# Kernel tuning notes

Hardware: AMD Instinct MI355X
Metric: run time of the kernel (lower is better)

Reference implementation:

```python
import jax, jax.numpy as jnp
import numpy as np

B, S, IN_F = 2, 2048, 1024
HEADS, DPH, OUT_F = 8, 64, 1024
ROOT_D = DPH ** 0.5


def setup_inputs() -> dict:
    key = jax.random.key(0)
    k1, k2, k3, k4, k5 = jax.random.split(key, 5)
    scale = 0.02
    return {
        "inputs": jax.random.normal(k1, (B, S, IN_F), dtype=jnp.float32),
        "Wq": jax.random.normal(k2, (IN_F, HEADS * DPH), dtype=jnp.float32) * scale,
        "Wk": jax.random.normal(k3, (IN_F, HEADS * DPH), dtype=jnp.float32) * scale,
        "Wv": jax.random.normal(k4, (IN_F, HEADS * DPH), dtype=jnp.float32) * scale,
        "Wo": jax.random.normal(k5, (DPH, OUT_F), dtype=jnp.float32) * scale,
        "bo": jnp.zeros((OUT_F,), dtype=jnp.float32),
    }


def reference(inputs, Wq, Wk, Wv, Wo, bo):
    b = inputs.shape[0]
    # Faithful to torch: raw view(b, heads, -1, d) reshape (NOT a transpose).
    q = (inputs @ Wq).reshape(b, HEADS, -1, DPH)  # [b, h, s, d]
    k = (inputs @ Wk).reshape(b, HEADS, -1, DPH)
    v = (inputs @ Wv).reshape(b, HEADS, -1, DPH)
    scores = jnp.einsum("bhqd,bhkd->bhqk", q, k)  # no pre-softmax scale
    attn = jax.nn.softmax(scores, axis=-1) / ROOT_D  # post-softmax scale (quirk)
    ctx = jnp.einsum("bhqk,bhkd->bhqd", attn, v)  # [b, h, s, d]
    # Per-head output projection d -> out_features; dropout p=0 is identity.
    return ctx @ Wo + bo  # [b, h, s, out_features]
```

## Files before the change

### kernel.cpp

```cpp
#include <hip/hip_runtime.h>


using short8  = __attribute__((ext_vector_type(8))) short;
using short4v = __attribute__((ext_vector_type(4))) short;
using f32x4   = __attribute__((ext_vector_type(4))) float;
using float4v = __attribute__((ext_vector_type(4))) float;
using uint4v  = __attribute__((ext_vector_type(4))) unsigned int;

__device__ __forceinline__ unsigned short f2bf(float x) {
  unsigned int u = __float_as_uint(x);
  u += 0x7FFFu + ((u >> 16) & 1u);
  return (unsigned short)(u >> 16);
}

#define GLD_LDS16(g, s)                                                              \
  __builtin_amdgcn_global_load_lds((const __attribute__((address_space(1))) unsigned int*)(g), \
                                   (__attribute__((address_space(3))) unsigned int*)(s), 16, 0, 0)

__global__ __launch_bounds__(256) void k_cvt(const float* __restrict__ in,
                                             unsigned short* __restrict__ out,
                                             int n4) {
  int id = blockIdx.x * 256 + threadIdx.x;
  if (id >= n4) return;
  float4v v = *(const float4v*)(in + (size_t)id * 4);
  short4v o;
#pragma unroll
  for (int i = 0; i < 4; ++i) o[i] = (short)f2bf(v[i]);
  *(short4v*)(out + (size_t)id * 4) = o;
}

__global__ __launch_bounds__(256) void k_twt3(const float* __restrict__ Wq,
                                              const float* __restrict__ Wk,
                                              const float* __restrict__ Wv,
                                              unsigned short* __restrict__ WT) {
  __shared__ alignas(16) unsigned short t[64][72];
  const int z = blockIdx.z;
  const float* W = (z == 0) ? Wq : (z == 1) ? Wk : Wv;
  unsigned short* dst0 = WT + (size_t)z * 524288;
  const int k0 = blockIdx.x * 64, n0 = blockIdx.y * 64;
  const int kk = threadIdx.x & 63, g = (threadIdx.x >> 6) * 16;
  const float* src = W + (size_t)(k0 + kk) * 512 + n0 + g;
#pragma unroll
  for (int j4 = 0; j4 < 4; ++j4) {
    float4v v = *(const float4v*)(src + j4 * 4);
#pragma unroll
    for (int i = 0; i < 4; ++i) t[g + j4 * 4 + i][kk] = f2bf(v[i]);
  }
  __syncthreads();
  const int nn = threadIdx.x >> 2, kg = (threadIdx.x & 3) * 16;
  short8 o0, o1;
#pragma unroll
  for (int j = 0; j < 8; ++j) { o0[j] = t[nn][kg + j]; o1[j] = t[nn][kg + 8 + j]; }
  unsigned short* dst = dst0 + (size_t)(n0 + nn) * 1024 + k0 + kg;
  *(short8*)dst = o0;
  *(short8*)(dst + 8) = o1;
}

__global__ __launch_bounds__(256) void k_twtO(const float* __restrict__ W,
                                              unsigned short* __restrict__ WT) {
  __shared__ alignas(16) unsigned short t[64][72];
  const int n0 = blockIdx.y * 64;
  const int kk = threadIdx.x & 63, g = (threadIdx.x >> 6) * 16;
  const float* src = W + (size_t)kk * 1024 + n0 + g;
#pragma unroll
  for (int j4 = 0; j4 < 4; ++j4) {
    float4v v = *(const float4v*)(src + j4 * 4);
#pragma unroll
    for (int i = 0; i < 4; ++i) t[g + j4 * 4 + i][kk] = f2bf(v[i]);
  }
  __syncthreads();
  const int nn = threadIdx.x >> 2, kg = (threadIdx.x & 3) * 16;
  short8 o0, o1;
#pragma unroll
  for (int j = 0; j < 8; ++j) { o0[j] = t[nn][kg + j]; o1[j] = t[nn][kg + 8 + j]; }
  unsigned short* dst = WT + (size_t)(n0 + nn) * 64 + kg;
  *(short8*)dst = o0;
  *(short8*)(dst + 8) = o1;
}

__global__ __launch_bounds__(256) void k_tv(const unsigned short* __restrict__ Vb,
                                            unsigned short* __restrict__ VT) {
  __shared__ alignas(16) unsigned short t[64][72];
  const int bh = blockIdx.y, r0 = blockIdx.x * 64;
  const int rr = threadIdx.x & 63, g = (threadIdx.x >> 6) * 16;
  const unsigned short* src = Vb + (size_t)bh * 131072 + (size_t)(r0 + rr) * 64 + g;
  short8 a = *(const short8*)src;
  short8 b = *(const short8*)(src + 8);
#pragma unroll
  for (int j = 0; j < 8; ++j) { t[g + j][rr] = a[j]; t[g + 8 + j][rr] = b[j]; }
  __syncthreads();
  const int d = threadIdx.x >> 2, rg = (threadIdx.x & 3) * 16;
  short8 o0, o1;
#pragma unroll
  for (int j = 0; j < 8; ++j) { o0[j] = t[d][rg + j]; o1[j] = t[d][rg + 8 + j]; }
  unsigned short* dst = VT + (size_t)bh * 131072 + (size_t)(r0 >> 6) * 4096 + d * 64 + rg;
  *(short8*)dst = o0;
  *(short8*)(dst + 8) = o1;
}

__global__ __launch_bounds__(256) void k_gemmqkv(const unsigned short* __restrict__ A,
                                                 const unsigned short* __restrict__ WT,
                                                 unsigned short* __restrict__ Q,
                                                 unsigned short* __restrict__ K_,
                                                 unsigned short* __restrict__ V_) {
  __shared__ alignas(16) unsigned short As[2][4096];
  __shared__ alignas(16) unsigned short Bs[2][8192];
  const int tid = threadIdx.x, w = tid >> 6, l = tid & 63;
  const int lr = l & 15, lg = l >> 4;
  const int m0 = blockIdx.x * 64;
  const int yy = blockIdx.y;
  const int wr = w >> 1, wc = w & 1;
  const unsigned short* ga = A  + (size_t)(m0 + w * 16 + (l >> 3)) * 1024 + (l & 7) * 8;
  const unsigned short* gb = WT + (size_t)(yy * 128 + w * 32 + (l >> 3)) * 1024 + (l & 7) * 8;

#pragma unroll
  for (int n = 0; n < 2; ++n) GLD_LDS16(ga + n * 8192, &As[0][w * 1024 + n * 512]);
#pragma unroll
  for (int n = 0; n < 4; ++n) GLD_LDS16(gb + n * 8192, &Bs[0][w * 2048 + n * 512]);
  asm volatile("s_waitcnt vmcnt(0)" ::: "memory");
  __syncthreads();

  f32x4 acc[2][4] = {};
  int cur = 0;
  for (int kt = 0; kt < 16; ++kt) {
    if (kt < 15) {
      const int k0 = (kt + 1) * 64;
#pragma unroll
      for (int n = 0; n < 2; ++n) GLD_LDS16(ga + n * 8192 + k0, &As[cur ^ 1][w * 1024 + n * 512]);
#pragma unroll
      for (int n = 0; n < 4; ++n) GLD_LDS16(gb + n * 8192 + k0, &Bs[cur ^ 1][w * 2048 + n * 512]);
    }
#pragma unroll
    for (int kk = 0; kk < 2; ++kk) {
      short8 a[2], b[4];
#pragma unroll
      for (int mi = 0; mi < 2; ++mi)
        a[mi] = *(const short8*)&As[cur][(wr * 32 + mi * 16 + lr) * 64 + kk * 32 + lg * 8];
#pragma unroll
      for (int ni = 0; ni < 4; ++ni)
        b[ni] = *(const short8*)&Bs[cur][(wc * 64 + ni * 16 + lr) * 64 + kk * 32 + lg * 8];
#pragma unroll
      for (int mi = 0; mi < 2; ++mi)
#pragma unroll
        for (int ni = 0; ni < 4; ++ni)
          acc[mi][ni] = __builtin_amdgcn_mfma_f32_16x16x32_bf16(a[mi], b[ni], acc[mi][ni], 0, 0, 0);
    }
    asm volatile("s_waitcnt vmcnt(0)" ::: "memory");
    __syncthreads();
    cur ^= 1;
  }
  const int which = yy >> 2;
  unsigned short* C = (which == 0) ? Q : (which == 1) ? K_ : V_;
  const int cbase = (yy & 3) * 128 + wc * 64;
#pragma unroll
  for (int mi = 0; mi < 2; ++mi)
#pragma unroll
    for (int ni = 0; ni < 4; ++ni) {
      int row = m0 + wr * 32 + mi * 16 + lg * 4;
      int col = cbase + ni * 16 + lr;
#pragma unroll
      for (int r = 0; r < 4; ++r)
        C[(size_t)(row + r) * 512 + col] = f2bf(acc[mi][ni][r]);
    }
}

__global__ __launch_bounds__(512) void k_attn(const unsigned short* __restrict__ Qb,
                                              const unsigned short* __restrict__ Kb,
                                              const unsigned short* __restrict__ VT,
                                              unsigned short* __restrict__ ctx) {
  __shared__ alignas(16) unsigned short Ks[2][8192];
  __shared__ alignas(16) unsigned short Vs[2][8192];
  __shared__ alignas(16) unsigned short Plds[8][16][128];
  const int tid = threadIdx.x, w = tid >> 6, l = tid & 63;
  const int lr = l & 15, lg = l >> 4;
  const int bid = blockIdx.x;
  const int xcd = bid & 7, j = bid >> 3;
  const int bh = xcd * 2 + (j >> 4);
  const int q0 = (j & 15) * 128;
  const int qrow = q0 + w * 16;
  const unsigned short* Qh  = Qb + (size_t)bh * 131072;
  const unsigned short* Kh  = Kb + (size_t)bh * 131072;
  const unsigned short* VTh = VT + (size_t)bh * 131072;

  short8 qb0 = *(const short8*)&Qh[(size_t)(qrow + lr) * 64 + lg * 8];
  short8 qb1 = *(const short8*)&Qh[(size_t)(qrow + lr) * 64 + 32 + lg * 8];

  const int srow = w * 8 + (l >> 3);
  const int scol = (((l & 7) ^ ((l >> 3) & 7)) << 3);
  const unsigned short* kps = Kh  + (size_t)srow * 64 + scol;
  const unsigned short* vps = VTh + (size_t)srow * 64 + scol;

#define STAGE(buf, it)                                                         \
  {                                                                            \
    _Pragma("unroll")                                                          \
    for (int sub = 0; sub < 2; ++sub) {                                        \
      GLD_LDS16(kps + (size_t)(2 * (it) + sub) * 4096, &Ks[buf][sub * 4096 + w * 512]); \
      GLD_LDS16(vps + (size_t)(2 * (it) + sub) * 4096, &Vs[buf][sub * 4096 + w * 512]); \
    }                                                                          \
  }

  f32x4 O[4] = {};
  float m_i = -1e30f, l_i = 0.f;

  STAGE(0, 0);
  asm volatile("s_waitcnt vmcnt(0)" ::: "memory");
  __syncthreads();

  const int fcol = ((lg ^ (lr & 7)) << 3);
  char* prow = (char*)&Plds[w][lr][0];
  int cur = 0;
  for (int it = 0; it < 16; ++it) {
    if (it < 15) STAGE(cur ^ 1, it + 1);
    f32x4 s[8] = {};
#pragma unroll
    for (int t = 0; t < 8; ++t) {
      const unsigned short* kRow = &Ks[cur][(t >> 2) * 4096 + ((t & 3) * 16 + lr) * 64];
      short8 ka = *(const short8*)(kRow + fcol);
      short8 kc = *(const short8*)(kRow + (fcol ^ 32));
      s[t] = __builtin_amdgcn_mfma_f32_16x16x32_bf16(ka, qb0, s[t], 0, 0, 0);
      s[t] = __builtin_amdgcn_mfma_f32_16x16x32_bf16(kc, qb1, s[t], 0, 0, 0);
    }
    short8 vf[4][4];
#pragma unroll
    for (int f = 0; f < 4; ++f) {
      const char* vRow0 = (const char*)&Vs[cur][(f * 16 + lr) * 64];
#pragma unroll
      for (int ks = 0; ks < 4; ++ks) {
        int ch = (((ks & 1) * 4 + lg) ^ (lr & 7));
        vf[f][ks] = *(const short8*)(vRow0 + (ks >> 1) * 8192 + ch * 16);
      }
    }
    float tm[8];
#pragma unroll
    for (int t = 0; t < 8; ++t)
      tm[t] = fmaxf(fmaxf(s[t][0], s[t][1]), fmaxf(s[t][2], s[t][3]));
    float tmax = fmaxf(fmaxf(fmaxf(tm[0], tm[1]), fmaxf(tm[2], tm[3])),
                       fmaxf(fmaxf(tm[4], tm[5]), fmaxf(tm[6], tm[7])));
    tmax = fmaxf(tmax, __shfl_xor(tmax, 16));
    tmax = fmaxf(tmax, __shfl_xor(tmax, 32));
    float mnew  = fmaxf(m_i, tmax);
    float alpha = __expf(m_i - mnew);
    float p[8][4];
#pragma unroll
    for (int t = 0; t < 8; ++t)
#pragma unroll
      for (int r = 0; r < 4; ++r) p[t][r] = __expf(s[t][r] - mnew);
    float us[8];
#pragma unroll
    for (int t = 0; t < 8; ++t)
      us[t] = (p[t][0] + p[t][1]) + (p[t][2] + p[t][3]);
    float ls = ((us[0] + us[1]) + (us[2] + us[3])) + ((us[4] + us[5]) + (us[6] + us[7]));
    ls += __shfl_xor(ls, 16);
    ls += __shfl_xor(ls, 32);
    l_i = l_i * alpha + ls;
    m_i = mnew;
#pragma unroll
    for (int f = 0; f < 4; ++f) O[f] *= alpha;
#pragma unroll
    for (int t = 0; t < 8; ++t) {
      short4v pk;
#pragma unroll
      for (int r = 0; r < 4; ++r) pk[r] = (short)f2bf(p[t][r]);
      int ch = ((2 * t + (lg >> 1)) ^ (lr & 7));
      *(short4v*)(prow + ch * 16 + (lg & 1) * 8) = pk;
    }
    asm volatile("s_waitcnt lgkmcnt(0)" ::: "memory");
    __builtin_amdgcn_sched_barrier(0);
    short8 pb[4];
#pragma unroll
    for (int ks = 0; ks < 4; ++ks)
      pb[ks] = *(const short8*)(prow + (((ks * 4 + lg) ^ (lr & 7)) << 4));
#pragma unroll
    for (int ks = 0; ks < 4; ++ks)
#pragma unroll
      for (int f = 0; f < 4; ++f)
        O[f] = __builtin_amdgcn_mfma_f32_16x16x32_bf16(vf[f][ks], pb[ks], O[f], 0, 0, 0);
    if (it < 15) {
      asm volatile("s_waitcnt vmcnt(0)" ::: "memory");
      __syncthreads();
    }
    cur ^= 1;
  }
  const float scale = 0.125f / l_i;
  unsigned short* base = ctx + (size_t)(bh * 2048 + qrow + lr) * 64;
#pragma unroll
  for (int f = 0; f < 4; ++f) {
    short4v o;
#pragma unroll
    for (int r = 0; r < 4; ++r) o[r] = (short)f2bf(O[f][r] * scale);
    *(short4v*)(base + f * 16 + lg * 4) = o;
  }
}

__global__ __launch_bounds__(256) void k_gemmo(const unsigned short* __restrict__ A,
                                               const unsigned short* __restrict__ BT,
                                               const float* __restrict__ bias,
                                               float* __restrict__ C) {
  __shared__ alignas(16) unsigned short As[128 * 64];
  __shared__ alignas(16) unsigned short Bs[128 * 64];
  const int tid = threadIdx.x, w = tid >> 6, l = tid & 63;
  const int lr = l & 15, lg = l >> 4;
  const int m0 = blockIdx.x * 128, n0 = blockIdx.y * 128;
  const int wr = w >> 1, wc = w & 1;
  const int srow = w * 8 + (l >> 3);
  const int scol = (l & 7) * 8;
  const unsigned short* ga = A  + (size_t)(m0 + srow) * 64 + scol;
  const unsigned short* gb = BT + (size_t)(n0 + srow) * 64 + scol;
#pragma unroll
  for (int i = 0; i < 4; ++i) {
    GLD_LDS16(ga + (size_t)i * 2048, As + (i * 32 + w * 8) * 64);
    GLD_LDS16(gb + (size_t)i * 2048, Bs + (i * 32 + w * 8) * 64);
  }
  asm volatile("s_waitcnt vmcnt(0)" ::: "memory");
  __syncthreads();
  f32x4 acc[4][4] = {};
#pragma unroll
  for (int kk = 0; kk < 2; ++kk) {
    short8 a[4], b[4];
#pragma unroll
    for (int mi = 0; mi < 4; ++mi)
      a[mi] = *(const short8*)&As[(wr * 64 + mi * 16 + lr) * 64 + kk * 32 + lg * 8];
#pragma unroll
    for (int ni = 0; ni < 4; ++ni)
      b[ni] = *(const short8*)&Bs[(wc * 64 + ni * 16 + lr) * 64 + kk * 32 + lg * 8];
#pragma unroll
    for (int mi = 0; mi < 4; ++mi)
#pragma unroll
      for (int ni = 0; ni < 4; ++ni)
        acc[mi][ni] = __builtin_amdgcn_mfma_f32_16x16x32_bf16(a[mi], b[ni], acc[mi][ni], 0, 0, 0);
  }
  float bv[4];
#pragma unroll
  for (int ni = 0; ni < 4; ++ni) bv[ni] = bias[n0 + wc * 64 + ni * 16 + lr];
#pragma unroll
  for (int mi = 0; mi < 4; ++mi)
#pragma unroll
    for (int ni = 0; ni < 4; ++ni) {
      int row = m0 + wr * 64 + mi * 16 + lg * 4;
      int col = n0 + wc * 64 + ni * 16 + lr;
#pragma unroll
      for (int r = 0; r < 4; ++r)
        C[(size_t)(row + r) * 1024 + col] = acc[mi][ni][r] + bv[ni];
    }
}

extern "C" void kernel_launch(void* const* d_in, const int* in_sizes, int n_in,
                              void* d_out, int out_size, void* d_ws, size_t ws_size,
                              hipStream_t stream) {
  const float* X  = (const float*)d_in[0];
  const float* Wq = (const float*)d_in[1];
  const float* Wk = (const float*)d_in[2];
  const float* Wv = (const float*)d_in[3];
  const float* Wo = (const float*)d_in[4];
  const float* bo = (const float*)d_in[5];
  float* out = (float*)d_out;

  char* ws = (char*)d_ws;
  unsigned short* Xb    = (unsigned short*)ws; ws += 8388608;
  unsigned short* WqkvT = (unsigned short*)ws; ws += 3145728;
  unsigned short* WoT   = (unsigned short*)ws; ws += 131072;
  unsigned short* Qb    = (unsigned short*)ws; ws += 4194304;
  unsigned short* Kb    = (unsigned short*)ws; ws += 4194304;
  unsigned short* Vb    = (unsigned short*)ws; ws += 4194304;
  unsigned short* VT    = (unsigned short*)ws; ws += 4194304;
  unsigned short* Cx    = (unsigned short*)ws; ws += 4194304;

  k_cvt<<<4096, 256, 0, stream>>>(X, Xb, 1048576);
  k_twt3<<<dim3(16, 8, 3), 256, 0, stream>>>(Wq, Wk, Wv, WqkvT);
  k_twtO<<<dim3(1, 16), 256, 0, stream>>>(Wo, WoT);

  k_gemmqkv<<<dim3(64, 12), 256, 0, stream>>>(Xb, WqkvT, Qb, Kb, Vb);

  k_tv<<<dim3(32, 16), 256, 0, stream>>>(Vb, VT);
  k_attn<<<256, 512, 0, stream>>>(Qb, Kb, VT, Cx);
  k_gemmo<<<dim3(256, 8), 256, 0, stream>>>(Cx, WoT, bo, out);
}
```

Baseline: 231.7 us.

## Enlarge QKV GEMM tile to 128x128 with swizzled LDS and MFMA priority hints

The QKV projection GEMM tile grows from 64x128 to 128x128 per block, doubling A-tile reuse per wave, and uses an XOR-swizzled LDS layout to avoid bank conflicts on fragment reads. s_setprio hints are placed around MFMA bursts in both the GEMM and the attention kernel, and the attention loop is unrolled by two. The cost is more accumulator registers and LDS per block and half as many GEMM blocks (384), which may lower occupancy or leave CUs underused.

```diff
diff --git a/kernel.cpp b/kernel.cpp
--- a/kernel.cpp
+++ b/kernel.cpp
@@ -103,47 +103,53 @@
                                                  unsigned short* __restrict__ Q,
                                                  unsigned short* __restrict__ K_,
                                                  unsigned short* __restrict__ V_) {
-  __shared__ alignas(16) unsigned short As[2][4096];
+  __shared__ alignas(16) unsigned short As[2][8192];
   __shared__ alignas(16) unsigned short Bs[2][8192];
   const int tid = threadIdx.x, w = tid >> 6, l = tid & 63;
   const int lr = l & 15, lg = l >> 4;
-  const int m0 = blockIdx.x * 64;
+  const int m0 = blockIdx.x * 128;
   const int yy = blockIdx.y;
   const int wr = w >> 1, wc = w & 1;
-  const unsigned short* ga = A  + (size_t)(m0 + w * 16 + (l >> 3)) * 1024 + (l & 7) * 8;
-  const unsigned short* gb = WT + (size_t)(yy * 128 + w * 32 + (l >> 3)) * 1024 + (l & 7) * 8;
-
-#pragma unroll
-  for (int n = 0; n < 2; ++n) GLD_LDS16(ga + n * 8192, &As[0][w * 1024 + n * 512]);
-#pragma unroll
-  for (int n = 0; n < 4; ++n) GLD_LDS16(gb + n * 8192, &Bs[0][w * 2048 + n * 512]);
+  const int srow = w * 8 + (l >> 3);
+  const int scol = (((l & 7) ^ ((l >> 3) & 7)) << 3);
+  const unsigned short* ga = A  + (size_t)(m0 + srow) * 1024 + scol;
+  const unsigned short* gb = WT + (size_t)(yy * 128 + srow) * 1024 + scol;
+
+#define QKV_STAGE(buf, k0)                                                     \
+  {                                                                            \
+    _Pragma("unroll")                                                          \
+    for (int i = 0; i < 4; ++i) {                                              \
+      GLD_LDS16(ga + (size_t)i * 32768 + (k0), &As[buf][(i * 32 + w * 8) * 64]); \
+      GLD_LDS16(gb + (size_t)i * 32768 + (k0), &Bs[buf][(i * 32 + w * 8) * 64]); \
+    }                                                                          \
+  }
+
+  QKV_STAGE(0, 0);
   asm volatile("s_waitcnt vmcnt(0)" ::: "memory");
   __syncthreads();
 
-  f32x4 acc[2][4] = {};
+  f32x4 acc[4][4] = {};
   int cur = 0;
   for (int kt = 0; kt < 16; ++kt) {
-    if (kt < 15) {
-      const int k0 = (kt + 1) * 64;
-#pragma unroll
-      for (int n = 0; n < 2; ++n) GLD_LDS16(ga + n * 8192 + k0, &As[cur ^ 1][w * 1024 + n * 512]);
-#pragma unroll
-      for (int n = 0; n < 4; ++n) GLD_LDS16(gb + n * 8192 + k0, &Bs[cur ^ 1][w * 2048 + n * 512]);
-    }
+    if (kt < 15) QKV_STAGE(cur ^ 1, (kt + 1) * 64);
 #pragma unroll
     for (int kk = 0; kk < 2; ++kk) {
-      short8 a[2], b[4];
-#pragma unroll
-      for (int mi = 0; mi < 2; ++mi)
-        a[mi] = *(const short8*)&As[cur][(wr * 32 + mi * 16 + lr) * 64 + kk * 32 + lg * 8];
+      short8 a[4], b[4];
+#pragma unroll
+      for (int mi = 0; mi < 4; ++mi)
+        a[mi] = *(const short8*)&As[cur][(wr * 64 + mi * 16 + lr) * 64 +
+                                         (((kk * 4 + lg) ^ (lr & 7)) << 3)];
 #pragma unroll
       for (int ni = 0; ni < 4; ++ni)
-        b[ni] = *(const short8*)&Bs[cur][(wc * 64 + ni * 16 + lr) * 64 + kk * 32 + lg * 8];
-#pragma unroll
-      for (int mi = 0; mi < 2; ++mi)
+        b[ni] = *(const short8*)&Bs[cur][(wc * 64 + ni * 16 + lr) * 64 +
+                                         (((kk * 4 + lg) ^ (lr & 7)) << 3)];
+      __builtin_amdgcn_s_setprio(1);
+#pragma unroll
+      for (int mi = 0; mi < 4; ++mi)
 #pragma unroll
         for (int ni = 0; ni < 4; ++ni)
           acc[mi][ni] = __builtin_amdgcn_mfma_f32_16x16x32_bf16(a[mi], b[ni], acc[mi][ni], 0, 0, 0);
+      __builtin_amdgcn_s_setprio(0);
     }
     asm volatile("s_waitcnt vmcnt(0)" ::: "memory");
     __syncthreads();
@@ -153,10 +159,10 @@
   unsigned short* C = (which == 0) ? Q : (which == 1) ? K_ : V_;
   const int cbase = (yy & 3) * 128 + wc * 64;
 #pragma unroll
-  for (int mi = 0; mi < 2; ++mi)
+  for (int mi = 0; mi < 4; ++mi)
 #pragma unroll
     for (int ni = 0; ni < 4; ++ni) {
-      int row = m0 + wr * 32 + mi * 16 + lg * 4;
+      int row = m0 + wr * 64 + mi * 16 + lg * 4;
       int col = cbase + ni * 16 + lr;
 #pragma unroll
       for (int r = 0; r < 4; ++r)
@@ -209,9 +215,11 @@
   const int fcol = ((lg ^ (lr & 7)) << 3);
   char* prow = (char*)&Plds[w][lr][0];
   int cur = 0;
+#pragma unroll 2
   for (int it = 0; it < 16; ++it) {
     if (it < 15) STAGE(cur ^ 1, it + 1);
     f32x4 s[8] = {};
+    __builtin_amdgcn_s_setprio(1);
 #pragma unroll
     for (int t = 0; t < 8; ++t) {
       const unsigned short* kRow = &Ks[cur][(t >> 2) * 4096 + ((t & 3) * 16 + lr) * 64];
@@ -220,6 +228,7 @@
       s[t] = __builtin_amdgcn_mfma_f32_16x16x32_bf16(ka, qb0, s[t], 0, 0, 0);
       s[t] = __builtin_amdgcn_mfma_f32_16x16x32_bf16(kc, qb1, s[t], 0, 0, 0);
     }
+    __builtin_amdgcn_s_setprio(0);
     short8 vf[4][4];
 #pragma unroll
     for (int f = 0; f < 4; ++f) {
@@ -270,11 +279,13 @@
 #pragma unroll
     for (int ks = 0; ks < 4; ++ks)
       pb[ks] = *(const short8*)(prow + (((ks * 4 + lg) ^ (lr & 7)) << 4));
+    __builtin_amdgcn_s_setprio(1);
 #pragma unroll
     for (int ks = 0; ks < 4; ++ks)
 #pragma unroll
       for (int f = 0; f < 4; ++f)
         O[f] = __builtin_amdgcn_mfma_f32_16x16x32_bf16(vf[f][ks], pb[ks], O[f], 0, 0, 0);
+    __builtin_amdgcn_s_setprio(0);
     if (it < 15) {
       asm volatile("s_waitcnt vmcnt(0)" ::: "memory");
       __syncthreads();
@@ -369,7 +380,7 @@
   k_twt3<<<dim3(16, 8, 3), 256, 0, stream>>>(Wq, Wk, Wv, WqkvT);
   k_twtO<<<dim3(1, 16), 256, 0, stream>>>(Wo, WoT);
 
-  k_gemmqkv<<<dim3(64, 12), 256, 0, stream>>>(Xb, WqkvT, Qb, Kb, Vb);
+  k_gemmqkv<<<dim3(32, 12), 256, 0, stream>>>(Xb, WqkvT, Qb, Kb, Vb);
 
   k_tv<<<dim3(32, 16), 256, 0, stream>>>(Vb, VT);
   k_attn<<<256, 512, 0, stream>>>(Qb, Kb, VT, Cx);
```

Result: faster. 226.4 us (-2.3%).
